# Kernel tuning notes

Hardware: AMD Instinct MI355X
Metric: run time of the kernel (lower is better)

Reference implementation:

```python
import jax, jax.numpy as jnp
import numpy as np

N_NODES = 20000
N_EDGES = 160000
N_GRAPHS = 64
HIDDEN = 128
CTX = 2048
HEADS = 4
NUM_LAYERS = 3
NUM_BINS = 240
MAX_DIST = 30.0
GAMMA = 0.5
BN_EPS = 1e-5
OUT_DIM = 1024


def setup_inputs() -> dict:
    key = jax.random.key(0)
    ks = jax.random.split(key, 32)
    inp = {}
    inp["atom_types"] = jax.random.randint(ks[0], (N_NODES,), 0, 118)
    inp["pos"] = jax.random.normal(ks[1], (N_NODES, 3), dtype=jnp.float32) * 5.0
    inp["edge_index"] = jax.random.randint(ks[2], (2, N_EDGES), 0, N_NODES)
    inp["edge_attr"] = jax.random.uniform(ks[3], (N_EDGES, 5), dtype=jnp.float32)
    inp["batch"] = jnp.sort(jax.random.randint(ks[4], (N_NODES,), 0, N_GRAPHS))
    inp["context_vector"] = jax.random.normal(ks[5], (N_GRAPHS, CTX), dtype=jnp.float32)
    # initial node embedding Linear(118 -> 128)
    inp["emb_W"] = jax.random.normal(ks[6], (118, HIDDEN), dtype=jnp.float32) * 0.05
    inp["emb_b"] = jnp.zeros((HIDDEN,), jnp.float32)
    # RBF positional MLP: Linear(720->128) + BN + ReLU + Linear(128->2048)
    inp["rbf_lin1_W"] = jax.random.normal(ks[7], (3 * NUM_BINS, 128), dtype=jnp.float32) * 0.03
    inp["rbf_lin1_b"] = jnp.zeros((128,), jnp.float32)
    inp["rbf_bn_g"] = jnp.ones((128,), jnp.float32)
    inp["rbf_bn_b"] = jnp.zeros((128,), jnp.float32)
    inp["rbf_bn_m"] = jax.random.normal(ks[8], (128,), dtype=jnp.float32) * 0.1
    inp["rbf_bn_v"] = jax.random.uniform(ks[9], (128,), dtype=jnp.float32, minval=0.5, maxval=1.5)
    inp["rbf_lin2_W"] = jax.random.normal(ks[10], (128, CTX), dtype=jnp.float32) * 0.05
    inp["rbf_lin2_b"] = jnp.zeros((CTX,), jnp.float32)
    # per-layer GAT params (stacked over layers)
    in_dim = HIDDEN + CTX  # 2176
    inp["gat_W"] = jax.random.normal(ks[11], (NUM_LAYERS, in_dim, HEADS * HIDDEN), dtype=jnp.float32) * 0.02
    inp["att_src"] = jax.random.normal(ks[12], (NUM_LAYERS, HEADS, HIDDEN), dtype=jnp.float32) * 0.1
    inp["att_dst"] = jax.random.normal(ks[13], (NUM_LAYERS, HEADS, HIDDEN), dtype=jnp.float32) * 0.1
    inp["gat_bias"] = jnp.zeros((NUM_LAYERS, HIDDEN), jnp.float32)
    inp["bn_g"] = jnp.ones((NUM_LAYERS, HIDDEN), jnp.float32)
    inp["bn_b"] = jnp.zeros((NUM_LAYERS, HIDDEN), jnp.float32)
    inp["bn_m"] = jax.random.normal(ks[14], (NUM_LAYERS, HIDDEN), dtype=jnp.float32) * 0.1
    inp["bn_v"] = jax.random.uniform(ks[15], (NUM_LAYERS, HIDDEN), dtype=jnp.float32, minval=0.5, maxval=1.5)
    # final Linear(128 -> 1024)
    inp["out_W"] = jax.random.normal(ks[16], (HIDDEN, OUT_DIM), dtype=jnp.float32) * 0.05
    inp["out_b"] = jnp.zeros((OUT_DIM,), jnp.float32)
    return inp


def _bn_eval(x, g, b, m, v):
    return (x - m) * jax.lax.rsqrt(v + BN_EPS) * g + b


def _forward(atom_types, pos, edge_index, edge_attr, batch, context_vector,
             emb_W, emb_b, rbf_lin1_W, rbf_lin1_b, rbf_bn_g, rbf_bn_b, rbf_bn_m,
             rbf_bn_v, rbf_lin2_W, rbf_lin2_b, gat_W, att_src, att_dst, gat_bias,
             bn_g, bn_b, bn_m, bn_v, out_W, out_b):
    N = atom_types.shape[0]
    # initial node embedding (one-hot @ W == row gather, but keep faithful math)
    x = jax.nn.one_hot(atom_types, 118, dtype=jnp.float32) @ emb_W + emb_b  # [N,128]
    # RBF positional encoding: [N,3,num_bins] -> [N,720]
    mu = jnp.linspace(-MAX_DIST, MAX_DIST, NUM_BINS, dtype=jnp.float32)
    rbf = jnp.exp(-GAMMA * (pos[..., None] - mu) ** 2).reshape(N, 3 * NUM_BINS)
    h = jax.nn.relu(_bn_eval(rbf @ rbf_lin1_W + rbf_lin1_b, rbf_bn_g, rbf_bn_b, rbf_bn_m, rbf_bn_v))
    pos_emb = h @ rbf_lin2_W + rbf_lin2_b  # [N,2048]
    context = context_vector[batch] + pos_emb  # pos_info == 'add'
    # GAT adds self-loops by default; edge_attr is ignored (edge_dim=None)
    loops = jnp.arange(N)
    src = jnp.concatenate([edge_index[0], loops])  # message source j
    dst = jnp.concatenate([edge_index[1], loops])  # message target i
    for l in range(NUM_LAYERS):
        xc = jnp.concatenate([x, context], axis=1)                  # [N,2176]
        xs = (xc @ gat_W[l]).reshape(N, HEADS, HIDDEN)              # [N,H,C]
        a_src = jnp.einsum('nhc,hc->nh', xs, att_src[l])            # [N,H]
        a_dst = jnp.einsum('nhc,hc->nh', xs, att_dst[l])
        alpha = jax.nn.leaky_relu(a_src[src] + a_dst[dst], 0.2)     # [E+N,H]
        amax = jax.ops.segment_max(alpha, dst, num_segments=N)
        alpha = jnp.exp(alpha - amax[dst])
        denom = jax.ops.segment_sum(alpha, dst, num_segments=N)
        alpha = alpha / jnp.maximum(denom[dst], 1e-16)
        msg = xs[src] * alpha[..., None]                             # [E+N,H,C]
        agg = jax.ops.segment_sum(msg, dst, num_segments=N)          # [N,H,C]
        x_conv = agg.mean(axis=1) + gat_bias[l]                      # concat=False -> head mean
        x_conv = _bn_eval(x_conv, bn_g[l], bn_b[l], bn_m[l], bn_v[l])
        x_conv = jax.nn.gelu(x_conv, approximate=False)
        x = x + x_conv                                               # residual; dropout inactive (eval)
    out = x @ out_W + out_b                                          # [N,1024]
    return jax.ops.segment_sum(out, batch, num_segments=N_GRAPHS)    # global_add_pool -> [B,1024]


def reference(atom_types, pos, edge_index, edge_attr, batch, context_vector,
              emb_W, emb_b, rbf_lin1_W, rbf_lin1_b, rbf_bn_g, rbf_bn_b, rbf_bn_m,
              rbf_bn_v, rbf_lin2_W, rbf_lin2_b, gat_W, att_src, att_dst, gat_bias,
              bn_g, bn_b, bn_m, bn_v, out_W, out_b):
    return _forward(atom_types, pos, edge_index, edge_attr, batch, context_vector,
                    emb_W, emb_b, rbf_lin1_W, rbf_lin1_b, rbf_bn_g, rbf_bn_b,
                    rbf_bn_m, rbf_bn_v, rbf_lin2_W, rbf_lin2_b, gat_W, att_src,
                    att_dst, gat_bias, bn_g, bn_b, bn_m, bn_v, out_W, out_b)
```

## Files before the change

### kernel.cpp

```cpp
#include <hip/hip_runtime.h>
#include <hip/hip_bf16.h>
#include <cstdint>

constexpr int HIDDEN = 128, CTXD = 2048, HEADS = 4, NLAYERS = 3;
constexpr int KRBF = 720, KPAD = 736;
constexpr int KXH = 256;

typedef __bf16 bf16x8 __attribute__((ext_vector_type(8)));
typedef float f32x4 __attribute__((ext_vector_type(4)));

static __device__ __forceinline__ unsigned short f2bf(float f) {
    union { float f; unsigned u; } v; v.f = f;
    unsigned r = v.u + 0x7fffu + ((v.u >> 16) & 1u);
    return (unsigned short)(r >> 16);
}
static __device__ __forceinline__ float bf2f(unsigned short s) {
    union { unsigned u; float f; } v; v.u = ((unsigned)s) << 16; return v.f;
}

__global__ __launch_bounds__(256) void k_tr(const float* __restrict__ src,
                                            unsigned short* __restrict__ dst,
                                            int R, int C) {
    __shared__ unsigned short t[32][34];
    int b = blockIdx.z;
    int c0 = blockIdx.x * 32, r0 = blockIdx.y * 32;
    const float* s = src + (size_t)b * R * C;
    unsigned short* d = dst + (size_t)b * R * C;
    for (int rr = threadIdx.y; rr < 32; rr += 8) {
        int r = r0 + rr, c = c0 + threadIdx.x;
        unsigned short val = 0;
        if (r < R && c < C) val = f2bf(s[(size_t)r * C + c]);
        t[rr][threadIdx.x] = val;
    }
    __syncthreads();
    for (int rr = threadIdx.y; rr < 32; rr += 8) {
        int c = c0 + rr, r = r0 + threadIdx.x;
        if (c < C && r < R) d[(size_t)c * R + r] = t[threadIdx.x][rr];
    }
}

__global__ __launch_bounds__(256) void k_w2bf(const float* __restrict__ W2,
                                              unsigned short* __restrict__ W2bf) {
    int i = blockIdx.x * 256 + threadIdx.x;
    if (i < 128 * CTXD) W2bf[i] = f2bf(W2[i]);
}
__global__ __launch_bounds__(256) void k_cpre(const float* __restrict__ ctx,
                                              const float* __restrict__ b2,
                                              unsigned short* __restrict__ cpre, int NG) {
    int i = blockIdx.x * 256 + threadIdx.x;
    if (i < NG * CTXD) cpre[i] = f2bf(ctx[i] + b2[i % CTXD]);
}
__global__ __launch_bounds__(256) void k_bccopy(const unsigned short* __restrict__ gatWt,
                                                unsigned short* __restrict__ Bc) {
    int i = blockIdx.x * 256 + threadIdx.x;
    if (i >= NLAYERS * 512 * 128) return;
    int lo = i >> 7, k = i & 127;
    Bc[(size_t)lo * KXH + k] = gatWt[(size_t)lo * 2176 + k];
}

__global__ __launch_bounds__(256) void k_embed(const int* __restrict__ at,
                                               const float* __restrict__ W,
                                               const float* __restrict__ b,
                                               float* __restrict__ x,
                                               unsigned short* __restrict__ xh, int N) {
    int i = blockIdx.x * 256 + threadIdx.x;
    if (i >= N * HIDDEN) return;
    int n = i >> 7, c = i & 127;
    float v = W[(size_t)at[n] * HIDDEN + c] + b[c];
    x[i] = v;
    xh[(size_t)n * KXH + c] = f2bf(v);
}

__global__ __launch_bounds__(256) void k_rbf_mfma(const float* __restrict__ pos,
                                                  const unsigned short* __restrict__ W1t,
                                                  const float* __restrict__ b1,
                                                  const float* __restrict__ g,
                                                  const float* __restrict__ bb,
                                                  const float* __restrict__ bm,
                                                  const float* __restrict__ bv,
                                                  unsigned short* __restrict__ xh, int N) {
    constexpr int LDT = 40;
    __shared__ unsigned short As[128 * LDT];
    __shared__ unsigned short Bs[128 * LDT];
    __shared__ float ps[128 * 3];
    const int tid = threadIdx.x;
    const int lane = tid & 63, wid = tid >> 6;
    const int nb = blockIdx.x * 128;
    for (int i = tid; i < 384; i += 256) {
        int n = nb + i / 3;
        ps[i] = (n < N) ? pos[(size_t)n * 3 + (i % 3)] : 1.0e9f;
    }
    __syncthreads();
    const int sr = tid >> 1, sk = (tid & 1) * 16;
    const int wr = (wid >> 1) * 64, wc = (wid & 1) * 64;
    const int fr = lane & 15, kg = lane >> 4;
    f32x4 acc[4][4];
#pragma unroll
    for (int i = 0; i < 4; i++)
#pragma unroll
        for (int j = 0; j < 4; j++)
#pragma unroll
            for (int r = 0; r < 4; r++) acc[i][j][r] = 0.f;
    const float p0 = ps[sr * 3], p1 = ps[sr * 3 + 1], p2 = ps[sr * 3 + 2];
    const unsigned short* bp = W1t + (size_t)sr * KPAD + sk;
    uint4 bv0 = *(const uint4*)bp, bv1 = *(const uint4*)(bp + 8);
    constexpr int NST = KPAD / 32;
    for (int ks = 0; ks < NST; ++ks) {
        unsigned short av[16];
#pragma unroll
        for (int j = 0; j < 16; j++) {
            int kglob = ks * 32 + sk + j;
            float v = 0.f;
            if (kglob < KRBF) {
                int d = kglob / 240, bin = kglob % 240;
                float mu = -30.f + (60.f / 239.f) * (float)bin;
                float p = (d == 0) ? p0 : ((d == 1) ? p1 : p2);
                float df = p - mu;
                v = __expf(-0.5f * df * df);
            }
            av[j] = f2bf(v);
        }
        __syncthreads();
        *(uint4*)&As[sr * LDT + sk] = *(const uint4*)&av[0];
        *(uint4*)&As[sr * LDT + sk + 8] = *(const uint4*)&av[8];
        *(uint4*)&Bs[sr * LDT + sk] = bv0;
        *(uint4*)&Bs[sr * LDT + sk + 8] = bv1;
        __syncthreads();
        if (ks + 1 < NST) {
            const unsigned short* bp2 = W1t + (size_t)sr * KPAD + (ks + 1) * 32 + sk;
            bv0 = *(const uint4*)bp2;
            bv1 = *(const uint4*)(bp2 + 8);
        }
        bf16x8 afr[4], bfr[4];
#pragma unroll
        for (int i = 0; i < 4; i++) {
            afr[i] = *reinterpret_cast<const bf16x8*>(&As[(wr + i * 16 + fr) * LDT + kg * 8]);
            bfr[i] = *reinterpret_cast<const bf16x8*>(&Bs[(wc + i * 16 + fr) * LDT + kg * 8]);
        }
#pragma unroll
        for (int i = 0; i < 4; i++)
#pragma unroll
            for (int j = 0; j < 4; j++)
                acc[i][j] = __builtin_amdgcn_mfma_f32_16x16x32_bf16(afr[i], bfr[j], acc[i][j], 0, 0, 0);
    }
    const int rg = lane >> 4;
#pragma unroll
    for (int i = 0; i < 4; i++) {
#pragma unroll
        for (int j = 0; j < 4; j++) {
            int col = wc + j * 16 + fr;
            float sc = g[col] * rsqrtf(bv[col] + 1e-5f);
            float sh = bb[col] - bm[col] * sc;
            float bc = b1[col];
#pragma unroll
            for (int r = 0; r < 4; r++) {
                int row = nb + wr + i * 16 + rg * 4 + r;
                if (row < N) {
                    float y = (acc[i][j][r] + bc) * sc + sh;
                    y = fmaxf(y, 0.f);
                    xh[(size_t)row * KXH + 128 + col] = f2bf(y);
                }
            }
        }
    }
}

__global__ __launch_bounds__(256) void k_trW1(const float* __restrict__ W1,
                                              unsigned short* __restrict__ W1t) {
    int i = blockIdx.x * 256 + threadIdx.x;
    if (i >= 128 * KPAD) return;
    int c = i / KPAD, k = i % KPAD;
    unsigned short v = 0;
    if (k < KRBF) v = f2bf(W1[(size_t)k * 128 + c]);
    W1t[i] = v;
}

template <int MODE>
__global__ __launch_bounds__(256) void k_gemm(const unsigned short* __restrict__ A, int lda, int M,
                                              const unsigned short* __restrict__ Bt, int ldb,
                                              int K,
                                              void* __restrict__ Cout, int ldc,
                                              const int* __restrict__ batch,
                                              const float* __restrict__ cw,
                                              long sA, long sB, long sC) {
    constexpr int LDT = 40;
    __shared__ unsigned short As[128 * LDT];
    __shared__ unsigned short Bs[128 * LDT];
    const int z = blockIdx.z;
    A += (size_t)z * sA;
    Bt += (size_t)z * sB;
    const int tid = threadIdx.x;
    const int lane = tid & 63, wid = tid >> 6;
    const int m0 = blockIdx.x * 128, n0 = blockIdx.y * 128;
    const int wr = (wid >> 1) * 64, wc = (wid & 1) * 64;
    const int sr = tid >> 1, sk = (tid & 1) * 16;
    f32x4 acc[4][4];
#pragma unroll
    for (int i = 0; i < 4; i++)
#pragma unroll
        for (int j = 0; j < 4; j++)
#pragma unroll
            for (int r = 0; r < 4; r++) acc[i][j][r] = 0.f;
    const int nst = K / 32;
    const int arow = min(m0 + sr, M - 1);
    const unsigned short* ap = A + (size_t)arow * lda + sk;
    const unsigned short* bp = Bt + (size_t)(n0 + sr) * ldb + sk;
    uint4 av0 = *(const uint4*)ap, av1 = *(const uint4*)(ap + 8);
    uint4 bv0 = *(const uint4*)bp, bv1 = *(const uint4*)(bp + 8);
    const int fr = lane & 15, kg = lane >> 4;
    for (int ks = 0; ks < nst; ++ks) {
        __syncthreads();
        *(uint4*)&As[sr * LDT + sk] = av0;
        *(uint4*)&As[sr * LDT + sk + 8] = av1;
        *(uint4*)&Bs[sr * LDT + sk] = bv0;
        *(uint4*)&Bs[sr * LDT + sk + 8] = bv1;
        __syncthreads();
        if (ks + 1 < nst) {
            const unsigned short* ap2 = A + (size_t)arow * lda + (ks + 1) * 32 + sk;
            const unsigned short* bp2 = Bt + (size_t)(n0 + sr) * ldb + (ks + 1) * 32 + sk;
            av0 = *(const uint4*)ap2; av1 = *(const uint4*)(ap2 + 8);
            bv0 = *(const uint4*)bp2; bv1 = *(const uint4*)(bp2 + 8);
        }
        bf16x8 afr[4], bfr[4];
#pragma unroll
        for (int i = 0; i < 4; i++) {
            afr[i] = *reinterpret_cast<const bf16x8*>(&As[(wr + i * 16 + fr) * LDT + kg * 8]);
            bfr[i] = *reinterpret_cast<const bf16x8*>(&Bs[(wc + i * 16 + fr) * LDT + kg * 8]);
        }
#pragma unroll
        for (int i = 0; i < 4; i++)
#pragma unroll
            for (int j = 0; j < 4; j++)
                acc[i][j] = __builtin_amdgcn_mfma_f32_16x16x32_bf16(afr[i], bfr[j], acc[i][j], 0, 0, 0);
    }
    const int rg = lane >> 4;
#pragma unroll
    for (int i = 0; i < 4; i++) {
#pragma unroll
        for (int j = 0; j < 4; j++) {
            int col = n0 + wc + j * 16 + fr;
#pragma unroll
            for (int r = 0; r < 4; r++) {
                int row = m0 + wr + i * 16 + rg * 4 + r;
                if (row < M) {
                    float vv = acc[i][j][r];
                    if (MODE == 2) {
                        ((float*)Cout)[(size_t)z * sC + (size_t)row * ldc + col] = vv;
                    } else if (MODE == 3) {
                        vv += cw[(size_t)batch[row] * 512 + col];
                        ((unsigned short*)Cout)[(size_t)row * ldc + col] = f2bf(vv);
                    } else {
                        ((unsigned short*)Cout)[(size_t)z * sC + (size_t)row * ldc + col] = f2bf(vv);
                    }
                }
            }
        }
    }
}

__global__ __launch_bounds__(256) void k_att(const unsigned short* __restrict__ xs,
                                             const float* __restrict__ att_s,
                                             const float* __restrict__ att_d,
                                             float* __restrict__ a_src,
                                             float* __restrict__ a_dst, int N) {
    int tid = threadIdx.x, lane = tid & 63, wid = tid >> 6;
    int n = blockIdx.x * 4 + wid;
    if (n >= N) return;
    int h = lane >> 4, c0 = (lane & 15) * 8;
    uint4 raw = *(const uint4*)(xs + (size_t)n * 512 + h * 128 + c0);
    const unsigned short* rs = (const unsigned short*)&raw;
    float ss = 0.f, sd = 0.f;
#pragma unroll
    for (int j = 0; j < 8; j++) {
        float xv = bf2f(rs[j]);
        ss += xv * att_s[h * 128 + c0 + j];
        sd += xv * att_d[h * 128 + c0 + j];
    }
#pragma unroll
    for (int d = 1; d < 16; d <<= 1) {
        ss += __shfl_xor(ss, d);
        sd += __shfl_xor(sd, d);
    }
    if ((lane & 15) == 0) {
        a_src[n * 4 + h] = ss;
        a_dst[n * 4 + h] = sd;
    }
}

__global__ void k_cnt_init(int* cnt, int N) {
    int i = blockIdx.x * 256 + threadIdx.x;
    if (i < N) cnt[i] = 1;
}
__global__ void k_cnt(const int* __restrict__ ei, int E, int* cnt) {
    int i = blockIdx.x * 256 + threadIdx.x;
    if (i < E) atomicAdd(&cnt[ei[E + i]], 1);
}
__global__ __launch_bounds__(1024) void k_scan(const int* __restrict__ cnt, int* __restrict__ rowptr,
                                               int* __restrict__ cursor, int n) {
    __shared__ int wsum[16];
    __shared__ int carry;
    int tid = threadIdx.x, lane = tid & 63, wid = tid >> 6;
    if (tid == 0) carry = 0;
    __syncthreads();
    for (int basei = 0; basei < n; basei += 1024) {
        int i = basei + tid;
        int v = (i < n) ? cnt[i] : 0;
        int s = v;
#pragma unroll
        for (int d = 1; d < 64; d <<= 1) {
            int t = __shfl_up(s, (unsigned)d);
            if (lane >= d) s += t;
        }
        if (lane == 63) wsum[wid] = s;
        __syncthreads();
        if (wid == 0 && lane < 16) {
            int ws = wsum[lane]; int t = ws;
#pragma unroll
            for (int d = 1; d < 16; d <<= 1) {
                int u = __shfl_up(t, (unsigned)d);
                if (lane >= d) t += u;
            }
            wsum[lane] = t - ws;
        }
        __syncthreads();
        int excl = carry + wsum[wid] + (s - v);
        if (i < n) { rowptr[i] = excl; cursor[i] = excl; }
        __syncthreads();
        if (tid == 1023) carry += wsum[15] + s;
        __syncthreads();
    }
    if (tid == 0) rowptr[n] = carry;
}
__global__ void k_fill(const int* __restrict__ ei, int E, int N, int* cursor, int* csrc) {
    int i = blockIdx.x * 256 + threadIdx.x;
    if (i >= E + N) return;
    int s, d;
    if (i < E) { s = ei[i]; d = ei[E + i]; }
    else { s = i - E; d = s; }
    int slot = atomicAdd(&cursor[d], 1);
    csrc[slot] = s;
}

__global__ __launch_bounds__(256) void k_agg(const int* __restrict__ rowptr,
                                             const int* __restrict__ csrc,
                                             const float* __restrict__ asrc,
                                             const float* __restrict__ adstv,
                                             const unsigned short* __restrict__ xs,
                                             const float* __restrict__ gbias,
                                             const float* __restrict__ bg,
                                             const float* __restrict__ bb,
                                             const float* __restrict__ bm,
                                             const float* __restrict__ bv,
                                             float* __restrict__ x,
                                             unsigned short* __restrict__ xh, int N) {
    int tid = threadIdx.x, lane = tid & 63, wid = tid >> 6;
    int n = blockIdx.x * 4 + wid;
    if (n >= N) return;
    int beg = rowptr[n], end = rowptr[n + 1];
    float ad[4];
#pragma unroll
    for (int hh = 0; hh < 4; hh++) ad[hh] = adstv[n * 4 + hh];
    float mx[4] = {-1e30f, -1e30f, -1e30f, -1e30f};
    for (int e = beg + lane; e < end; e += 64) {
        int s = csrc[e];
#pragma unroll
        for (int hh = 0; hh < 4; hh++) {
            float a = asrc[s * 4 + hh] + ad[hh];
            a = a > 0.f ? a : 0.2f * a;
            mx[hh] = fmaxf(mx[hh], a);
        }
    }
#pragma unroll
    for (int d = 1; d < 64; d <<= 1)
#pragma unroll
        for (int hh = 0; hh < 4; hh++) mx[hh] = fmaxf(mx[hh], __shfl_xor(mx[hh], d));
    float sm[4] = {0.f, 0.f, 0.f, 0.f};
    for (int e = beg + lane; e < end; e += 64) {
        int s = csrc[e];
#pragma unroll
        for (int hh = 0; hh < 4; hh++) {
            float a = asrc[s * 4 + hh] + ad[hh];
            a = a > 0.f ? a : 0.2f * a;
            sm[hh] += __expf(a - mx[hh]);
        }
    }
#pragma unroll
    for (int d = 1; d < 64; d <<= 1)
#pragma unroll
        for (int hh = 0; hh < 4; hh++) sm[hh] += __shfl_xor(sm[hh], d);
    int h = lane >> 4, c0 = (lane & 15) * 8;
    float am = mx[h], iv = 1.f / fmaxf(sm[h], 1e-16f), adh = ad[h];
    float acc[8];
#pragma unroll
    for (int j = 0; j < 8; j++) acc[j] = 0.f;
    for (int e = beg; e < end; e++) {
        int s = csrc[e];
        float a = asrc[s * 4 + h] + adh;
        a = a > 0.f ? a : 0.2f * a;
        float w = __expf(a - am) * iv;
        uint4 raw = *(const uint4*)(xs + (size_t)s * 512 + h * 128 + c0);
        const unsigned short* rs = (const unsigned short*)&raw;
#pragma unroll
        for (int j = 0; j < 8; j++) acc[j] += w * bf2f(rs[j]);
    }
#pragma unroll
    for (int j = 0; j < 8; j++) {
        acc[j] += __shfl_xor(acc[j], 16);
        acc[j] += __shfl_xor(acc[j], 32);
    }
    if (lane < 16) {
#pragma unroll
        for (int j = 0; j < 8; j++) {
            int c = c0 + j;
            float t = acc[j] * 0.25f + gbias[c];
            float sc = bg[c] * rsqrtf(bv[c] + 1e-5f);
            float y = (t - bm[c]) * sc + bb[c];
            float ge = 0.5f * y * (1.f + erff(y * 0.70710678118f));
            float xn = x[(size_t)n * 128 + c] + ge;
            x[(size_t)n * 128 + c] = xn;
            xh[(size_t)n * KXH + c] = f2bf(xn);
        }
    }
}

__global__ __launch_bounds__(256) void k_pool(const float* __restrict__ x,
                                              const int* __restrict__ batch,
                                              const float* __restrict__ W,
                                              const float* __restrict__ bo,
                                              float* __restrict__ out, int N) {
    __shared__ float xg[128];
    __shared__ float tmp[256];
    __shared__ int bounds[2];
    int g = blockIdx.x, tid = threadIdx.x;
    if (tid < 2) {
        int key = g + tid, lo = 0, hi = N;
        while (lo < hi) { int mid = (lo + hi) >> 1; if (batch[mid] < key) lo = mid + 1; else hi = mid; }
        bounds[tid] = lo;
    }
    __syncthreads();
    int s = bounds[0], e = bounds[1];
    int c = tid & 127, rgp = tid >> 7;
    float a = 0.f;
    for (int n = s + rgp; n < e; n += 2) a += x[(size_t)n * 128 + c];
    tmp[tid] = a;
    __syncthreads();
    if (tid < 128) xg[tid] = tmp[tid] + tmp[tid + 128];
    __syncthreads();
    float cntf = (float)(e - s);
    for (int j = tid; j < 1024; j += 256) {
        float o = cntf * bo[j];
        for (int cc = 0; cc < 128; cc++) o += xg[cc] * W[(size_t)cc * 1024 + j];
        out[(size_t)g * 1024 + j] = o;
    }
}

extern "C" void kernel_launch(void* const* d_in, const int* in_sizes, int n_in,
                              void* d_out, int out_size, void* d_ws, size_t ws_size,
                              hipStream_t stream) {
    const int N = in_sizes[0];
    const int E = in_sizes[2] / 2;
    const int NG = in_sizes[5] / CTXD;
    const int* at = (const int*)d_in[0];
    const float* pos = (const float*)d_in[1];
    const int* ei = (const int*)d_in[2];
    const int* batch = (const int*)d_in[4];
    const float* ctx = (const float*)d_in[5];
    const float* embW = (const float*)d_in[6];
    const float* embB = (const float*)d_in[7];
    const float* W1 = (const float*)d_in[8];
    const float* b1 = (const float*)d_in[9];
    const float* rg = (const float*)d_in[10];
    const float* rb = (const float*)d_in[11];
    const float* rm = (const float*)d_in[12];
    const float* rv = (const float*)d_in[13];
    const float* W2 = (const float*)d_in[14];
    const float* b2 = (const float*)d_in[15];
    const float* gatW = (const float*)d_in[16];
    const float* atts = (const float*)d_in[17];
    const float* attd = (const float*)d_in[18];
    const float* gbias = (const float*)d_in[19];
    const float* bg = (const float*)d_in[20];
    const float* bbb = (const float*)d_in[21];
    const float* bm = (const float*)d_in[22];
    const float* bv = (const float*)d_in[23];
    const float* outW = (const float*)d_in[24];
    const float* outb = (const float*)d_in[25];
    float* out = (float*)d_out;

    char* basep = (char*)d_ws;
    size_t off = 0;
    auto alloc = [&](size_t bytes) -> char* {
        char* p = basep + off;
        off = (off + bytes + 255) & ~(size_t)255;
        return p;
    };
    unsigned short* xh = (unsigned short*)alloc((size_t)N * KXH * 2);
    float* x = (float*)alloc((size_t)N * 128 * 4);
    unsigned short* xs = (unsigned short*)alloc((size_t)N * 512 * 2);
    float* a_src = (float*)alloc((size_t)N * 4 * 4);
    float* a_dst = (float*)alloc((size_t)N * 4 * 4);
    int* cnt = (int*)alloc((size_t)N * 4);
    int* rowptr = (int*)alloc((size_t)(N + 1) * 4);
    int* cursor = (int*)alloc((size_t)N * 4);
    int* csrc = (int*)alloc((size_t)(E + N) * 4);
    unsigned short* gatWt = (unsigned short*)alloc((size_t)NLAYERS * 512 * 2176 * 2);
    unsigned short* W1t = (unsigned short*)alloc((size_t)128 * KPAD * 2);
    unsigned short* W2bf = (unsigned short*)alloc((size_t)128 * CTXD * 2);
    unsigned short* cpre = (unsigned short*)alloc((size_t)NG * CTXD * 2);
    unsigned short* Bc = (unsigned short*)alloc((size_t)NLAYERS * 512 * KXH * 2);
    float* cW = (float*)alloc((size_t)NLAYERS * NG * 512 * 4);
    (void)ws_size; (void)n_in; (void)out_size;

    {
        dim3 b(32, 8);
        dim3 g1((512 + 31) / 32, (2176 + 31) / 32, NLAYERS);
        k_tr<<<g1, b, 0, stream>>>(gatW, gatWt, 2176, 512);
        k_trW1<<<(128 * KPAD + 255) / 256, 256, 0, stream>>>(W1, W1t);
        k_w2bf<<<(128 * CTXD + 255) / 256, 256, 0, stream>>>(W2, W2bf);
        k_cpre<<<(NG * CTXD + 255) / 256, 256, 0, stream>>>(ctx, b2, cpre, NG);
        k_bccopy<<<(NLAYERS * 512 * 128 + 255) / 256, 256, 0, stream>>>(gatWt, Bc);
        dim3 gm(4, 1, NLAYERS);
        k_gemm<0><<<gm, 256, 0, stream>>>(gatWt + 128, 2176, 512, W2bf, CTXD, CTXD,
                                          Bc + 128, KXH, nullptr, nullptr,
                                          (long)512 * 2176, 0, (long)512 * KXH);
        dim3 gc(1, 4, NLAYERS);
        k_gemm<2><<<gc, 256, 0, stream>>>(cpre, CTXD, NG, gatWt + 128, 2176, CTXD,
                                          cW, 512, nullptr, nullptr,
                                          0, (long)512 * 2176, (long)NG * 512);
    }
    k_embed<<<(N * 128 + 255) / 256, 256, 0, stream>>>(at, embW, embB, x, xh, N);
    k_rbf_mfma<<<(N + 127) / 128, 256, 0, stream>>>(pos, W1t, b1, rg, rb, rm, rv, xh, N);
    k_cnt_init<<<(N + 255) / 256, 256, 0, stream>>>(cnt, N);
    k_cnt<<<(E + 255) / 256, 256, 0, stream>>>(ei, E, cnt);
    k_scan<<<1, 1024, 0, stream>>>(cnt, rowptr, cursor, N);
    k_fill<<<(E + N + 255) / 256, 256, 0, stream>>>(ei, E, N, cursor, csrc);
    {
        dim3 g((N + 127) / 128, 4, 1);
        for (int l = 0; l < NLAYERS; l++) {
            k_gemm<3><<<g, 256, 0, stream>>>(xh, KXH, N, Bc + (size_t)l * 512 * KXH, KXH, KXH,
                                             xs, 512, batch, cW + (size_t)l * NG * 512,
                                             0, 0, 0);
            k_att<<<(N + 3) / 4, 256, 0, stream>>>(xs, atts + l * HEADS * 128, attd + l * HEADS * 128,
                                                   a_src, a_dst, N);
            k_agg<<<(N + 3) / 4, 256, 0, stream>>>(rowptr, csrc, a_src, a_dst, xs,
                                                   gbias + l * 128, bg + l * 128, bbb + l * 128,
                                                   bm + l * 128, bv + l * 128, x, xh, N);
        }
    }
    k_pool<<<NG, 256, 0, stream>>>(x, batch, outW, outb, out, N);
}
```

Before: 508.5 us.

## Merge prep GEMMs into one launch and rewrite GAT aggregation with online softmax

The two batched precompute GEMMs now run as a single k_prep launch, dispatching on blockIdx.z, and the layer GEMM gets a dedicated k_gemm3 wrapper with constant strides. The aggregation kernel replaces its two-pass max/sum over edges with a single chunked online-softmax pass using float4 loads of the attention scores. Each chunk's per-edge weights and source indices are staged in shared memory so the feature gather can be unrolled two edges at a time. For nodes with at most 64 in-edges, the weights are reused from registers instead of recomputed. This cuts redundant gathers of csrc and asrc and one launch, at the cost of extra shuffle reductions per chunk and some idle blocks in the merged launch.

```diff
diff --git a/kernel.cpp b/kernel.cpp
--- a/kernel.cpp
+++ b/kernel.cpp
@@ -56,6 +56,16 @@
     if (i >= NLAYERS * 512 * 128) return;
     int lo = i >> 7, k = i & 127;
     Bc[(size_t)lo * KXH + k] = gatWt[(size_t)lo * 2176 + k];
+}
+
+__global__ __launch_bounds__(256) void k_trW1(const float* __restrict__ W1,
+                                              unsigned short* __restrict__ W1t) {
+    int i = blockIdx.x * 256 + threadIdx.x;
+    if (i >= 128 * KPAD) return;
+    int c = i / KPAD, k = i % KPAD;
+    unsigned short v = 0;
+    if (k < KRBF) v = f2bf(W1[(size_t)k * 128 + c]);
+    W1t[i] = v;
 }
 
 __global__ __launch_bounds__(256) void k_embed(const int* __restrict__ at,
@@ -165,33 +175,17 @@
     }
 }
 
-__global__ __launch_bounds__(256) void k_trW1(const float* __restrict__ W1,
-                                              unsigned short* __restrict__ W1t) {
-    int i = blockIdx.x * 256 + threadIdx.x;
-    if (i >= 128 * KPAD) return;
-    int c = i / KPAD, k = i % KPAD;
-    unsigned short v = 0;
-    if (k < KRBF) v = f2bf(W1[(size_t)k * 128 + c]);
-    W1t[i] = v;
-}
-
 template <int MODE>
-__global__ __launch_bounds__(256) void k_gemm(const unsigned short* __restrict__ A, int lda, int M,
-                                              const unsigned short* __restrict__ Bt, int ldb,
-                                              int K,
-                                              void* __restrict__ Cout, int ldc,
-                                              const int* __restrict__ batch,
-                                              const float* __restrict__ cw,
-                                              long sA, long sB, long sC) {
+__device__ __forceinline__ void gemm_core(unsigned short* As, unsigned short* Bs,
+                                          const unsigned short* __restrict__ A, int lda, int M,
+                                          const unsigned short* __restrict__ Bt, int ldb, int K,
+                                          void* __restrict__ Cout, int ldc,
+                                          const int* __restrict__ batch,
+                                          const float* __restrict__ cw,
+                                          int m0, int n0) {
     constexpr int LDT = 40;
-    __shared__ unsigned short As[128 * LDT];
-    __shared__ unsigned short Bs[128 * LDT];
-    const int z = blockIdx.z;
-    A += (size_t)z * sA;
-    Bt += (size_t)z * sB;
     const int tid = threadIdx.x;
     const int lane = tid & 63, wid = tid >> 6;
-    const int m0 = blockIdx.x * 128, n0 = blockIdx.y * 128;
     const int wr = (wid >> 1) * 64, wc = (wid & 1) * 64;
     const int sr = tid >> 1, sk = (tid & 1) * 16;
     f32x4 acc[4][4];
@@ -245,16 +239,50 @@
                 if (row < M) {
                     float vv = acc[i][j][r];
                     if (MODE == 2) {
-                        ((float*)Cout)[(size_t)z * sC + (size_t)row * ldc + col] = vv;
+                        ((float*)Cout)[(size_t)row * ldc + col] = vv;
                     } else if (MODE == 3) {
                         vv += cw[(size_t)batch[row] * 512 + col];
                         ((unsigned short*)Cout)[(size_t)row * ldc + col] = f2bf(vv);
                     } else {
-                        ((unsigned short*)Cout)[(size_t)z * sC + (size_t)row * ldc + col] = f2bf(vv);
+                        ((unsigned short*)Cout)[(size_t)row * ldc + col] = f2bf(vv);
                     }
                 }
             }
         }
+    }
+}
+
+__global__ __launch_bounds__(256) void k_gemm3(const unsigned short* __restrict__ A, int M,
+                                               const unsigned short* __restrict__ Bt,
+                                               unsigned short* __restrict__ C,
+                                               const int* __restrict__ batch,
+                                               const float* __restrict__ cw) {
+    constexpr int LDT = 40;
+    __shared__ unsigned short As[128 * LDT];
+    __shared__ unsigned short Bs[128 * LDT];
+    gemm_core<3>(As, Bs, A, KXH, M, Bt, KXH, KXH, C, 512, batch, cw,
+                 blockIdx.x * 128, blockIdx.y * 128);
+}
+
+__global__ __launch_bounds__(256) void k_prep(const unsigned short* __restrict__ gatWt,
+                                              const unsigned short* __restrict__ W2bf,
+                                              const unsigned short* __restrict__ cpre,
+                                              unsigned short* __restrict__ Bc,
+                                              float* __restrict__ cW, int NG) {
+    constexpr int LDT = 40;
+    __shared__ unsigned short As[128 * LDT];
+    __shared__ unsigned short Bs[128 * LDT];
+    int z = blockIdx.z;
+    if (z < 3) {
+        if (blockIdx.y != 0) return;
+        gemm_core<0>(As, Bs, gatWt + (size_t)z * 512 * 2176 + 128, 2176, 512,
+                     W2bf, CTXD, CTXD, Bc + (size_t)z * 512 * KXH + 128, KXH,
+                     nullptr, nullptr, blockIdx.x * 128, 0);
+    } else {
+        if (blockIdx.x != 0) return;
+        int zz = z - 3;
+        gemm_core<2>(As, Bs, cpre, CTXD, NG, gatWt + (size_t)zz * 512 * 2176 + 128, 2176, CTXD,
+                     cW + (size_t)zz * NG * 512, 512, nullptr, nullptr, 0, blockIdx.y * 128);
     }
 }
 
@@ -353,55 +381,106 @@
                                              const float* __restrict__ bv,
                                              float* __restrict__ x,
                                              unsigned short* __restrict__ xh, int N) {
+    __shared__ float wsh[4][64][4];
+    __shared__ int ssh[4][64];
     int tid = threadIdx.x, lane = tid & 63, wid = tid >> 6;
     int n = blockIdx.x * 4 + wid;
     if (n >= N) return;
     int beg = rowptr[n], end = rowptr[n + 1];
-    float ad[4];
-#pragma unroll
-    for (int hh = 0; hh < 4; hh++) ad[hh] = adstv[n * 4 + hh];
-    float mx[4] = {-1e30f, -1e30f, -1e30f, -1e30f};
-    for (int e = beg + lane; e < end; e += 64) {
-        int s = csrc[e];
-#pragma unroll
-        for (int hh = 0; hh < 4; hh++) {
-            float a = asrc[s * 4 + hh] + ad[hh];
-            a = a > 0.f ? a : 0.2f * a;
-            mx[hh] = fmaxf(mx[hh], a);
-        }
-    }
-#pragma unroll
-    for (int d = 1; d < 64; d <<= 1)
-#pragma unroll
-        for (int hh = 0; hh < 4; hh++) mx[hh] = fmaxf(mx[hh], __shfl_xor(mx[hh], d));
-    float sm[4] = {0.f, 0.f, 0.f, 0.f};
-    for (int e = beg + lane; e < end; e += 64) {
-        int s = csrc[e];
-#pragma unroll
-        for (int hh = 0; hh < 4; hh++) {
-            float a = asrc[s * 4 + hh] + ad[hh];
-            a = a > 0.f ? a : 0.2f * a;
-            sm[hh] += __expf(a - mx[hh]);
-        }
-    }
-#pragma unroll
-    for (int d = 1; d < 64; d <<= 1)
-#pragma unroll
-        for (int hh = 0; hh < 4; hh++) sm[hh] += __shfl_xor(sm[hh], d);
-    int h = lane >> 4, c0 = (lane & 15) * 8;
-    float am = mx[h], iv = 1.f / fmaxf(sm[h], 1e-16f), adh = ad[h];
+    float4 ad = *(const float4*)(adstv + (size_t)n * 4);
+    int nch = (end - beg + 63) >> 6;
+    float m0 = -1e30f, m1 = -1e30f, m2 = -1e30f, m3 = -1e30f;
+    float s0 = 0.f, s1 = 0.f, s2 = 0.f, s3 = 0.f;
+    float a0 = -1e30f, a1 = -1e30f, a2 = -1e30f, a3 = -1e30f;
+    int sv = 0;
+    for (int base = beg; base < end; base += 64) {
+        int idx = base + lane;
+        float b0 = -1e30f, b1 = -1e30f, b2 = -1e30f, b3 = -1e30f;
+        int s = 0;
+        if (idx < end) {
+            s = csrc[idx];
+            float4 t = *(const float4*)(asrc + (size_t)s * 4);
+            b0 = t.x + ad.x; b0 = b0 > 0.f ? b0 : 0.2f * b0;
+            b1 = t.y + ad.y; b1 = b1 > 0.f ? b1 : 0.2f * b1;
+            b2 = t.z + ad.z; b2 = b2 > 0.f ? b2 : 0.2f * b2;
+            b3 = t.w + ad.w; b3 = b3 > 0.f ? b3 : 0.2f * b3;
+        }
+        float c0 = b0, c1 = b1, c2 = b2, c3 = b3;
+#pragma unroll
+        for (int d = 1; d < 64; d <<= 1) {
+            c0 = fmaxf(c0, __shfl_xor(c0, d));
+            c1 = fmaxf(c1, __shfl_xor(c1, d));
+            c2 = fmaxf(c2, __shfl_xor(c2, d));
+            c3 = fmaxf(c3, __shfl_xor(c3, d));
+        }
+        float nm0 = fmaxf(m0, c0), nm1 = fmaxf(m1, c1), nm2 = fmaxf(m2, c2), nm3 = fmaxf(m3, c3);
+        float e0 = (idx < end) ? __expf(b0 - nm0) : 0.f;
+        float e1 = (idx < end) ? __expf(b1 - nm1) : 0.f;
+        float e2 = (idx < end) ? __expf(b2 - nm2) : 0.f;
+        float e3 = (idx < end) ? __expf(b3 - nm3) : 0.f;
+#pragma unroll
+        for (int d = 1; d < 64; d <<= 1) {
+            e0 += __shfl_xor(e0, d); e1 += __shfl_xor(e1, d);
+            e2 += __shfl_xor(e2, d); e3 += __shfl_xor(e3, d);
+        }
+        s0 = s0 * __expf(m0 - nm0) + e0; m0 = nm0;
+        s1 = s1 * __expf(m1 - nm1) + e1; m1 = nm1;
+        s2 = s2 * __expf(m2 - nm2) + e2; m2 = nm2;
+        s3 = s3 * __expf(m3 - nm3) + e3; m3 = nm3;
+        a0 = b0; a1 = b1; a2 = b2; a3 = b3; sv = s;
+    }
+    float i0 = 1.f / fmaxf(s0, 1e-16f), i1 = 1.f / fmaxf(s1, 1e-16f);
+    float i2 = 1.f / fmaxf(s2, 1e-16f), i3 = 1.f / fmaxf(s3, 1e-16f);
+    const int h = lane >> 4, c0i = (lane & 15) * 8;
     float acc[8];
 #pragma unroll
     for (int j = 0; j < 8; j++) acc[j] = 0.f;
-    for (int e = beg; e < end; e++) {
-        int s = csrc[e];
-        float a = asrc[s * 4 + h] + adh;
-        a = a > 0.f ? a : 0.2f * a;
-        float w = __expf(a - am) * iv;
-        uint4 raw = *(const uint4*)(xs + (size_t)s * 512 + h * 128 + c0);
-        const unsigned short* rs = (const unsigned short*)&raw;
-#pragma unroll
-        for (int j = 0; j < 8; j++) acc[j] += w * bf2f(rs[j]);
+    for (int base = beg; base < end; base += 64) {
+        int s; float w0, w1, w2, w3;
+        if (nch == 1) {
+            s = sv;
+            w0 = __expf(a0 - m0) * i0; w1 = __expf(a1 - m1) * i1;
+            w2 = __expf(a2 - m2) * i2; w3 = __expf(a3 - m3) * i3;
+        } else {
+            int idx = base + lane;
+            float b0 = -1e30f, b1 = -1e30f, b2 = -1e30f, b3 = -1e30f;
+            s = 0;
+            if (idx < end) {
+                s = csrc[idx];
+                float4 t = *(const float4*)(asrc + (size_t)s * 4);
+                b0 = t.x + ad.x; b0 = b0 > 0.f ? b0 : 0.2f * b0;
+                b1 = t.y + ad.y; b1 = b1 > 0.f ? b1 : 0.2f * b1;
+                b2 = t.z + ad.z; b2 = b2 > 0.f ? b2 : 0.2f * b2;
+                b3 = t.w + ad.w; b3 = b3 > 0.f ? b3 : 0.2f * b3;
+            }
+            w0 = __expf(b0 - m0) * i0; w1 = __expf(b1 - m1) * i1;
+            w2 = __expf(b2 - m2) * i2; w3 = __expf(b3 - m3) * i3;
+        }
+        ssh[wid][lane] = s;
+        wsh[wid][lane][0] = w0; wsh[wid][lane][1] = w1;
+        wsh[wid][lane][2] = w2; wsh[wid][lane][3] = w3;
+        int cnt = min(64, end - base);
+        int i = 0;
+        for (; i + 2 <= cnt; i += 2) {
+            int sa = ssh[wid][i], sb = ssh[wid][i + 1];
+            float wa = wsh[wid][i][h], wb = wsh[wid][i + 1][h];
+            uint4 ra = *(const uint4*)(xs + ((size_t)sa << 9) + (h << 7) + c0i);
+            uint4 rb = *(const uint4*)(xs + ((size_t)sb << 9) + (h << 7) + c0i);
+            const unsigned short* qa = (const unsigned short*)&ra;
+            const unsigned short* qb = (const unsigned short*)&rb;
+#pragma unroll
+            for (int j = 0; j < 8; j++) acc[j] += wa * bf2f(qa[j]);
+#pragma unroll
+            for (int j = 0; j < 8; j++) acc[j] += wb * bf2f(qb[j]);
+        }
+        if (i < cnt) {
+            int sa = ssh[wid][i];
+            float wa = wsh[wid][i][h];
+            uint4 ra = *(const uint4*)(xs + ((size_t)sa << 9) + (h << 7) + c0i);
+            const unsigned short* qa = (const unsigned short*)&ra;
+#pragma unroll
+            for (int j = 0; j < 8; j++) acc[j] += wa * bf2f(qa[j]);
+        }
     }
 #pragma unroll
     for (int j = 0; j < 8; j++) {
@@ -411,7 +490,7 @@
     if (lane < 16) {
 #pragma unroll
         for (int j = 0; j < 8; j++) {
-            int c = c0 + j;
+            int c = c0i + j;
             float t = acc[j] * 0.25f + gbias[c];
             float sc = bg[c] * rsqrtf(bv[c] + 1e-5f);
             float y = (t - bm[c]) * sc + bb[c];
@@ -519,14 +598,8 @@
         k_w2bf<<<(128 * CTXD + 255) / 256, 256, 0, stream>>>(W2, W2bf);
         k_cpre<<<(NG * CTXD + 255) / 256, 256, 0, stream>>>(ctx, b2, cpre, NG);
         k_bccopy<<<(NLAYERS * 512 * 128 + 255) / 256, 256, 0, stream>>>(gatWt, Bc);
-        dim3 gm(4, 1, NLAYERS);
-        k_gemm<0><<<gm, 256, 0, stream>>>(gatWt + 128, 2176, 512, W2bf, CTXD, CTXD,
-                                          Bc + 128, KXH, nullptr, nullptr,
-                                          (long)512 * 2176, 0, (long)512 * KXH);
-        dim3 gc(1, 4, NLAYERS);
-        k_gemm<2><<<gc, 256, 0, stream>>>(cpre, CTXD, NG, gatWt + 128, 2176, CTXD,
-                                          cW, 512, nullptr, nullptr,
-                                          0, (long)512 * 2176, (long)NG * 512);
+        dim3 gp(4, 4, 6);
+        k_prep<<<gp, 256, 0, stream>>>(gatWt, W2bf, cpre, Bc, cW, NG);
     }
     k_embed<<<(N * 128 + 255) / 256, 256, 0, stream>>>(at, embW, embB, x, xh, N);
     k_rbf_mfma<<<(N + 127) / 128, 256, 0, stream>>>(pos, W1t, b1, rg, rb, rm, rv, xh, N);
@@ -537,9 +610,8 @@
     {
         dim3 g((N + 127) / 128, 4, 1);
         for (int l = 0; l < NLAYERS; l++) {
-            k_gemm<3><<<g, 256, 0, stream>>>(xh, KXH, N, Bc + (size_t)l * 512 * KXH, KXH, KXH,
-                                             xs, 512, batch, cW + (size_t)l * NG * 512,
-                                             0, 0, 0);
+            k_gemm3<<<g, 256, 0, stream>>>(xh, N, Bc + (size_t)l * 512 * KXH,
+                                           xs, batch, cW + (size_t)l * NG * 512);
             k_att<<<(N + 3) / 4, 256, 0, stream>>>(xs, atts + l * HEADS * 128, attd + l * HEADS * 128,
                                                    a_src, a_dst, N);
             k_agg<<<(N + 3) / 4, 256, 0, stream>>>(rowptr, csrc, a_src, a_dst, xs,
```

New measurement: 472.1 us. 7.2% less time.
